# Kernel optimization log

Hardware: AMD Instinct MI355X
Metric: run time of the kernel (lower is better)

## Reference

```python
import jax, jax.numpy as jnp
import numpy as np

J = 24  # fixed pooling window (SampleLength/N = 1200/50)


def setup_inputs() -> dict:
    key = jax.random.key(0)
    k1, k2, k3 = jax.random.split(key, 3)
    T, N, K, C = 786432, 50, 400, 10  # T = 32768 segments * J
    x = jax.random.normal(k1, (T, N), dtype=jnp.float32)
    W1 = jax.random.normal(k2, (K, N), dtype=jnp.float32) * 0.1
    W2 = jax.random.normal(k3, (C, K), dtype=jnp.float32) * 0.1
    return {"x": x, "W1": W1, "W2": W2}


def reference(x, W1, W2):
    # linear + relu: [T, N] @ [N, K] -> [T, K]
    local_features = jax.nn.relu(jnp.einsum('tn,kn->tk', x, W1))
    # fixed-window mean over consecutive J rows: [T, K] -> [T//J, K]
    T, K = local_features.shape
    features = local_features.reshape(T // J, J, K).mean(axis=1)
    # final linear: [T//J, K] @ [K, C] -> [T//J, C]
    logits = jnp.einsum('bk,ck->bc', features, W2)
    return logits
```

## Files before the change

### kernel.cpp

```cpp
#include <hip/hip_runtime.h>
#include <hip/hip_bf16.h>

#define T_TOTAL 786432
#define N_IN 50
#define K_FEAT 400
#define C_OUT 10
#define NSEG 32768

#define W1F_TASKS (25 * 2 * 64)
#define W2T_OFF_BYTES 51200
#define W2T_FLOATS (25 * 320)
#define W2F_OFF_BYTES 83200
#define W2F_TASKS (13 * 64)
#define W1F32_OFF_BYTES 98304
#define W1F32_TASKS (13 * 4 * 64)
#define PREP_TASKS (W1F_TASKS + W2T_FLOATS + W2F_TASKS + W1F32_TASKS)
#define POOLED_OFF_BYTES 163840
#define POOLED_STRIDE 416
#define WS_NEEDED (POOLED_OFF_BYTES + (size_t)NSEG * POOLED_STRIDE * 2)

typedef __bf16 bfx8 __attribute__((ext_vector_type(8)));
typedef short  s16x8 __attribute__((ext_vector_type(8)));
typedef float  f32x4 __attribute__((ext_vector_type(4)));
typedef float  f32x16 __attribute__((ext_vector_type(16)));

static __device__ __forceinline__ short f2bf(float f) {
    union { float f; unsigned u; } v; v.f = f;
    unsigned r = v.u + 0x7fffu + ((v.u >> 16) & 1u);
    return (short)(r >> 16);
}

__global__ void prep_kernel(const float* __restrict__ W1,
                            const float* __restrict__ W2,
                            short* __restrict__ w1f, float* __restrict__ w2t,
                            short* __restrict__ w2f, short* __restrict__ w1f32)
{
    const int gid = blockIdx.x * blockDim.x + threadIdx.x;
    if (gid < W1F_TASKS) {
        const int lane = gid & 63;
        const int s    = (gid >> 6) & 1;
        const int tile = gid >> 7;
        const int m16  = lane & 15;
        const int quad = lane >> 4;
        const float* row = W1 + (tile * 16 + m16) * N_IN;
        s16x8 v;
        #pragma unroll
        for (int j = 0; j < 8; ++j) {
            const int n = s * 32 + quad * 8 + j;
            v[j] = (n < N_IN) ? f2bf(row[n]) : (short)0;
        }
        *(s16x8*)&w1f[gid * 8] = v;
    } else if (gid < W1F_TASKS + W2T_FLOATS) {
        const int i   = gid - W1F_TASKS;
        const int j   = i / 320;
        const int tid = i - j * 320;
        const int o    = tid >> 4;
        const int part = tid & 15;
        const int seg  = (o >= 10) ? 1 : 0;
        const int cls  = o - seg * 10;
        w2t[i] = W2[cls * K_FEAT + part * 25 + j];
    } else if (gid < W1F_TASKS + W2T_FLOATS + W2F_TASKS) {
        const int i    = gid - W1F_TASKS - W2T_FLOATS;
        const int lane = i & 63;
        const int kt   = i >> 6;
        const int m16  = lane & 15;
        const int quad = lane >> 4;
        s16x8 v;
        #pragma unroll
        for (int j = 0; j < 8; ++j) {
            const int feat = kt * 32 + quad * 8 + j;
            v[j] = (m16 < C_OUT && feat < K_FEAT) ? f2bf(W2[m16 * K_FEAT + feat])
                                                  : (short)0;
        }
        *(s16x8*)&w2f[i * 8] = v;
    } else if (gid < PREP_TASKS) {
        const int i    = gid - W1F_TASKS - W2T_FLOATS - W2F_TASKS;
        const int lane = i & 63;
        const int fi   = i >> 6;
        const int ft   = fi >> 2;
        const int kt   = fi & 3;
        const int feat = ft * 32 + (lane & 31);
        const int cbase = kt * 16 + (lane >> 5) * 8;
        s16x8 v;
        #pragma unroll
        for (int j = 0; j < 8; ++j) {
            const int col = cbase + j;
            v[j] = (feat < K_FEAT && col < N_IN) ? f2bf(W1[feat * N_IN + col])
                                                 : (short)0;
        }
        *(s16x8*)&w1f32[i * 8] = v;
    }
}

__global__ __launch_bounds__(256, 4) void phase1_kernel(
    const float* __restrict__ x, const short* __restrict__ w1f32,
    short* __restrict__ pooled)
{
    const int tid  = threadIdx.x;
    const int lane = tid & 63;
    const int m32  = lane & 31;
    const int h    = lane >> 5;
    const int chunk = blockIdx.x * 4 + (tid >> 6);
    const s16x8* wf = (const s16x8*)w1f32;

    s16x8 Af[3][4];
    {
        const float* xg = x + (size_t)chunk * (96 * N_IN);
        #pragma unroll
        for (int rt = 0; rt < 3; ++rt) {
            const float* rp = xg + (32 * rt + m32) * N_IN;
            #pragma unroll
            for (int kt = 0; kt < 3; ++kt) {
                const float* p = rp + 16 * kt + 8 * h;
                s16x8 f;
                #pragma unroll
                for (int q = 0; q < 4; ++q) {
                    const float2 u = *(const float2*)(p + 2 * q);
                    f[2 * q]     = f2bf(u.x);
                    f[2 * q + 1] = f2bf(u.y);
                }
                Af[rt][kt] = f;
            }
            s16x8 f3 = {0, 0, 0, 0, 0, 0, 0, 0};
            if (h == 0) {
                const float2 u = *(const float2*)(rp + 48);
                f3[0] = f2bf(u.x); f3[1] = f2bf(u.y);
            }
            Af[rt][3] = f3;
        }
    }

    const int segbase = chunk * 4;

    s16x8 Bc[4], Bn[4];
    #pragma unroll
    for (int kt = 0; kt < 4; ++kt) Bc[kt] = wf[kt * 64 + lane];

    for (int ft = 0; ft < 13; ++ft) {
        const int ftn = (ft < 12) ? ft + 1 : 12;
        #pragma unroll
        for (int kt = 0; kt < 4; ++kt) Bn[kt] = wf[(ftn * 4 + kt) * 64 + lane];

        float s0 = 0.f, s1 = 0.f, s2 = 0.f, s3 = 0.f;
        #pragma unroll
        for (int rt = 0; rt < 3; ++rt) {
            f32x16 acc;
            #pragma unroll
            for (int r = 0; r < 16; ++r) acc[r] = 0.f;
            #pragma unroll
            for (int kt = 0; kt < 4; ++kt)
                acc = __builtin_amdgcn_mfma_f32_32x32x16_bf16(
                        __builtin_bit_cast(bfx8, Af[rt][kt]),
                        __builtin_bit_cast(bfx8, Bc[kt]), acc, 0, 0, 0);
            float c0 = 0.f, c1 = 0.f;
            #pragma unroll
            for (int r = 0; r < 16; ++r) {
                const float v = fmaxf(acc[r], 0.f);
                if ((r >> 2) < 3 - rt) c0 += v; else c1 += v;
            }
            if (rt == 0)      { s0 += c0; s1 += c1; }
            else if (rt == 1) { s1 += c0; s2 += c1; }
            else              { s2 += c0; s3 += c1; }
        }
        s0 += __shfl_xor(s0, 32);
        s1 += __shfl_xor(s1, 32);
        s2 += __shfl_xor(s2, 32);
        s3 += __shfl_xor(s3, 32);
        if (lane < 32) {
            const size_t fo = 32 * ft + lane;
            pooled[(size_t)(segbase + 0) * POOLED_STRIDE + fo] = f2bf(s0);
            pooled[(size_t)(segbase + 1) * POOLED_STRIDE + fo] = f2bf(s1);
            pooled[(size_t)(segbase + 2) * POOLED_STRIDE + fo] = f2bf(s2);
            pooled[(size_t)(segbase + 3) * POOLED_STRIDE + fo] = f2bf(s3);
        }
        #pragma unroll
        for (int kt = 0; kt < 4; ++kt) Bc[kt] = Bn[kt];
    }
}

__global__ __launch_bounds__(256) void phase2_kernel(
    const short* __restrict__ pooled, const short* __restrict__ w2f,
    float* __restrict__ out)
{
    const int tid  = threadIdx.x;
    const int lane = tid & 63;
    const int m16  = lane & 15;
    const int quad = lane >> 4;
    const int segbase = (blockIdx.x * 4 + (tid >> 6)) * 16;
    const s16x8* wf = (const s16x8*)w2f;
    const short* arow = pooled + (size_t)(segbase + m16) * POOLED_STRIDE;

    f32x4 acc = {0.f, 0.f, 0.f, 0.f};
    s16x8 zero = {0, 0, 0, 0, 0, 0, 0, 0};
    #pragma unroll
    for (int kt = 0; kt < 13; ++kt) {
        const s16x8 b = wf[kt * 64 + lane];
        const s16x8 a = (kt == 12 && quad >= 2)
                            ? zero
                            : *(const s16x8*)(arow + kt * 32 + quad * 8);
        acc = __builtin_amdgcn_mfma_f32_16x16x32_bf16(
                __builtin_bit_cast(bfx8, a), __builtin_bit_cast(bfx8, b),
                acc, 0, 0, 0);
    }
    if (m16 < C_OUT) {
        #pragma unroll
        for (int rg = 0; rg < 4; ++rg)
            out[(size_t)(segbase + quad * 4 + rg) * C_OUT + m16] =
                acc[rg] * (1.0f / 24.0f);
    }
}

#define FB_CPB 4
#define FB_NTHREADS 320
#define FB_XS_STRIDE 72
#define FB_XS_ROWS (FB_CPB * 48)

__global__ __launch_bounds__(FB_NTHREADS) void classifier_fb(
    const float* __restrict__ x, const short* __restrict__ w1f,
    const float* __restrict__ w2t, float* __restrict__ out)
{
    __shared__ short xs[FB_XS_ROWS * FB_XS_STRIDE];
    __shared__ float pooled[2 * K_FEAT];

    const int tid  = threadIdx.x;
    const int wave = tid >> 6;
    const int lane = tid & 63;
    const int m16  = lane & 15;
    const int quad = lane >> 4;

    {
        const float* xb = x + (size_t)blockIdx.x * (FB_XS_ROWS * N_IN);
        #pragma unroll
        for (int it = 0; it < (FB_XS_ROWS * 25) / FB_NTHREADS; ++it) {
            const int i = tid + it * FB_NTHREADS;
            const int r = i / 25;
            const int c2 = i - r * 25;
            const float2 v = *(const float2*)(xb + 2 * i);
            const int packed = (unsigned short)f2bf(v.x) |
                               ((unsigned)(unsigned short)f2bf(v.y) << 16);
            *(int*)&xs[r * FB_XS_STRIDE + 2 * c2] = packed;
        }
        for (int i = tid; i < FB_XS_ROWS * 7; i += FB_NTHREADS) {
            const int r = i / 7;
            const int c = 50 + 2 * (i - r * 7);
            *(int*)&xs[r * FB_XS_STRIDE + c] = 0;
        }
    }

    s16x8 bfrag[5][2];
    {
        const s16x8* wf = (const s16x8*)w1f;
        #pragma unroll
        for (int t = 0; t < 5; ++t)
            #pragma unroll
            for (int s = 0; s < 2; ++s)
                bfrag[t][s] = wf[((wave * 5 + t) * 2 + s) * 64 + lane];
    }

    const int o    = tid >> 4;
    const int part = tid & 15;
    const int segO = (o >= 10) ? 1 : 0;
    const int cls  = o - segO * 10;
    float w2r[25];
    #pragma unroll
    for (int j = 0; j < 25; ++j) w2r[j] = w2t[j * FB_NTHREADS + tid];

    __syncthreads();

    for (int ciq = 0; ciq < FB_CPB; ++ciq) {
        s16x8 a[3][2];
        #pragma unroll
        for (int r = 0; r < 3; ++r) {
            const short* arow =
                &xs[(ciq * 48 + r * 16 + m16) * FB_XS_STRIDE + quad * 8];
            a[r][0] = *(const s16x8*)(arow);
            a[r][1] = *(const s16x8*)(arow + 32);
        }
        #pragma unroll
        for (int t = 0; t < 5; ++t) {
            float c0 = 0.f, c1 = 0.f;
            #pragma unroll
            for (int r = 0; r < 3; ++r) {
                f32x4 acc = {0.f, 0.f, 0.f, 0.f};
                acc = __builtin_amdgcn_mfma_f32_16x16x32_bf16(
                        __builtin_bit_cast(bfx8, a[r][0]),
                        __builtin_bit_cast(bfx8, bfrag[t][0]), acc, 0, 0, 0);
                acc = __builtin_amdgcn_mfma_f32_16x16x32_bf16(
                        __builtin_bit_cast(bfx8, a[r][1]),
                        __builtin_bit_cast(bfx8, bfrag[t][1]), acc, 0, 0, 0);
                const float s = fmaxf(acc[0], 0.f) + fmaxf(acc[1], 0.f)
                              + fmaxf(acc[2], 0.f) + fmaxf(acc[3], 0.f);
                if (r * 4 + quad < 6) c0 += s; else c1 += s;
            }
            c0 += __shfl_xor(c0, 16); c0 += __shfl_xor(c0, 32);
            c1 += __shfl_xor(c1, 16); c1 += __shfl_xor(c1, 32);
            if (quad == 0) {
                const int feat = (wave * 5 + t) * 16 + m16;
                pooled[feat] = c0;
                pooled[K_FEAT + feat] = c1;
            }
        }
        __syncthreads();

        float sum = 0.f;
        const float* pv = &pooled[segO * K_FEAT + part * 25];
        #pragma unroll
        for (int j = 0; j < 25; ++j) sum += pv[j] * w2r[j];
        sum += __shfl_down(sum, 8, 16);
        sum += __shfl_down(sum, 4, 16);
        sum += __shfl_down(sum, 2, 16);
        sum += __shfl_down(sum, 1, 16);
        if (part == 0) {
            const int chunk = blockIdx.x * FB_CPB + ciq;
            out[(chunk * 2 + segO) * C_OUT + cls] = sum * (1.0f / 24.0f);
        }
        __syncthreads();
    }
}

extern "C" void kernel_launch(void* const* d_in, const int* in_sizes, int n_in,
                              void* d_out, int out_size, void* d_ws, size_t ws_size,
                              hipStream_t stream) {
    const float* x  = (const float*)d_in[0];
    const float* W1 = (const float*)d_in[1];
    const float* W2 = (const float*)d_in[2];
    float* out = (float*)d_out;

    short* w1f   = (short*)d_ws;
    float* w2t   = (float*)((char*)d_ws + W2T_OFF_BYTES);
    short* w2f   = (short*)((char*)d_ws + W2F_OFF_BYTES);
    short* w1f32 = (short*)((char*)d_ws + W1F32_OFF_BYTES);
    short* pooled = (short*)((char*)d_ws + POOLED_OFF_BYTES);

    prep_kernel<<<(PREP_TASKS + 255) / 256, 256, 0, stream>>>(W1, W2, w1f, w2t,
                                                              w2f, w1f32);

    if (ws_size >= WS_NEEDED) {
        phase1_kernel<<<2048, 256, 0, stream>>>(x, w1f32, pooled);
        phase2_kernel<<<512, 256, 0, stream>>>(pooled, w2f, out);
    } else {
        classifier_fb<<<4096, FB_NTHREADS, 0, stream>>>(x, w1f, w2t, out);
    }
}
```

Measured before the change: 260.7 us.

## Fuse classifier into phase1 and stage x through LDS with packed bf16 convert

Drops the pooled intermediate buffer and the separate phase2 kernel. Each wave now multiplies its pooled sums by fp32 W2 slices and reduces across lanes with shuffles before writing the logits. The x tile is loaded with coalesced float4 reads, converted with v_cvt_pk_bf16_f32, staged in LDS, and then read back as MFMA fragments. This saves a global round trip and a kernel launch. In exchange it adds 38KB of LDS per block, which may limit occupancy, plus extra FMA and shuffle work.

```diff
diff --git a/kernel.cpp b/kernel.cpp
--- a/kernel.cpp
+++ b/kernel.cpp
@@ -10,14 +10,12 @@
 #define W1F_TASKS (25 * 2 * 64)
 #define W2T_OFF_BYTES 51200
 #define W2T_FLOATS (25 * 320)
-#define W2F_OFF_BYTES 83200
-#define W2F_TASKS (13 * 64)
 #define W1F32_OFF_BYTES 98304
 #define W1F32_TASKS (13 * 4 * 64)
-#define PREP_TASKS (W1F_TASKS + W2T_FLOATS + W2F_TASKS + W1F32_TASKS)
-#define POOLED_OFF_BYTES 163840
-#define POOLED_STRIDE 416
-#define WS_NEEDED (POOLED_OFF_BYTES + (size_t)NSEG * POOLED_STRIDE * 2)
+#define W2P_OFF_BYTES 163840
+#define W2P_TASKS (13 * 64)
+#define PREP_TASKS (W1F_TASKS + W2T_FLOATS + W1F32_TASKS + W2P_TASKS)
+#define WS_NEEDED (W2P_OFF_BYTES + (size_t)W2P_TASKS * 8 * 4)
 
 typedef __bf16 bfx8 __attribute__((ext_vector_type(8)));
 typedef short  s16x8 __attribute__((ext_vector_type(8)));
@@ -33,7 +31,7 @@
 __global__ void prep_kernel(const float* __restrict__ W1,
                             const float* __restrict__ W2,
                             short* __restrict__ w1f, float* __restrict__ w2t,
-                            short* __restrict__ w2f, short* __restrict__ w1f32)
+                            short* __restrict__ w1f32, float* __restrict__ w2p)
 {
     const int gid = blockIdx.x * blockDim.x + threadIdx.x;
     if (gid < W1F_TASKS) {
@@ -59,22 +57,8 @@
         const int seg  = (o >= 10) ? 1 : 0;
         const int cls  = o - seg * 10;
         w2t[i] = W2[cls * K_FEAT + part * 25 + j];
-    } else if (gid < W1F_TASKS + W2T_FLOATS + W2F_TASKS) {
+    } else if (gid < W1F_TASKS + W2T_FLOATS + W1F32_TASKS) {
         const int i    = gid - W1F_TASKS - W2T_FLOATS;
-        const int lane = i & 63;
-        const int kt   = i >> 6;
-        const int m16  = lane & 15;
-        const int quad = lane >> 4;
-        s16x8 v;
-        #pragma unroll
-        for (int j = 0; j < 8; ++j) {
-            const int feat = kt * 32 + quad * 8 + j;
-            v[j] = (m16 < C_OUT && feat < K_FEAT) ? f2bf(W2[m16 * K_FEAT + feat])
-                                                  : (short)0;
-        }
-        *(s16x8*)&w2f[i * 8] = v;
-    } else if (gid < PREP_TASKS) {
-        const int i    = gid - W1F_TASKS - W2T_FLOATS - W2F_TASKS;
         const int lane = i & 63;
         const int fi   = i >> 6;
         const int ft   = fi >> 2;
@@ -89,48 +73,83 @@
                                                  : (short)0;
         }
         *(s16x8*)&w1f32[i * 8] = v;
+    } else if (gid < PREP_TASKS) {
+        const int i    = gid - W1F_TASKS - W2T_FLOATS - W1F32_TASKS;
+        const int lane = i & 63;
+        const int ft   = i >> 6;
+        const int m32  = lane & 31;
+        const int h    = lane >> 5;
+        const int feat = 32 * ft + m32;
+        float v[8];
+        #pragma unroll
+        for (int c = 0; c < 8; ++c)
+            v[c] = (c < 5 && feat < K_FEAT) ? W2[(h * 5 + c) * K_FEAT + feat]
+                                            : 0.f;
+        float4* dst = (float4*)&w2p[(size_t)i * 8];
+        dst[0] = make_float4(v[0], v[1], v[2], v[3]);
+        dst[1] = make_float4(v[4], v[5], v[6], v[7]);
     }
 }
 
 __global__ __launch_bounds__(256, 4) void phase1_kernel(
     const float* __restrict__ x, const short* __restrict__ w1f32,
-    short* __restrict__ pooled)
+    const float* __restrict__ w2p, float* __restrict__ out)
 {
+    __shared__ __align__(16) short xs[4 * 4800];
     const int tid  = threadIdx.x;
     const int lane = tid & 63;
+    const int wv   = tid >> 6;
     const int m32  = lane & 31;
     const int h    = lane >> 5;
-    const int chunk = blockIdx.x * 4 + (tid >> 6);
+    const int chunk = blockIdx.x * 4 + wv;
+    short* myxs = xs + wv * 4800;
+
+    {
+        const float* xg = x + (size_t)chunk * 4800;
+        #pragma unroll
+        for (int i = 0; i < 19; ++i) {
+            const int q = 64 * i + lane;
+            if (i < 18 || lane < 48) {
+                const float4 v = *(const float4*)(xg + 4 * q);
+                int lo, hi;
+                asm("v_cvt_pk_bf16_f32 %0, %1, %2" : "=v"(lo) : "v"(v.x), "v"(v.y));
+                asm("v_cvt_pk_bf16_f32 %0, %1, %2" : "=v"(hi) : "v"(v.z), "v"(v.w));
+                int2 pk; pk.x = lo; pk.y = hi;
+                *(int2*)&myxs[4 * q] = pk;
+            }
+        }
+    }
+    asm volatile("s_waitcnt lgkmcnt(0)" ::: "memory");
+    __builtin_amdgcn_sched_barrier(0);
+
+    s16x8 Af[3][4];
+    #pragma unroll
+    for (int rt = 0; rt < 3; ++rt) {
+        const int row = 32 * rt + m32;
+        const short* rp = myxs + row * 50 + 8 * h;
+        #pragma unroll
+        for (int kt = 0; kt < 3; ++kt) {
+            int d0 = *(const int*)(rp + 16 * kt + 0);
+            int d1 = *(const int*)(rp + 16 * kt + 2);
+            int d2 = *(const int*)(rp + 16 * kt + 4);
+            int d3 = *(const int*)(rp + 16 * kt + 6);
+            int4 di = {d0, d1, d2, d3};
+            Af[rt][kt] = __builtin_bit_cast(s16x8, di);
+        }
+        int dt = 0;
+        if (h == 0) dt = *(const int*)(myxs + row * 50 + 48);
+        int4 di3 = {dt, 0, 0, 0};
+        Af[rt][3] = __builtin_bit_cast(s16x8, di3);
+    }
+
+    const int segbase = chunk * 4;
     const s16x8* wf = (const s16x8*)w1f32;
 
-    s16x8 Af[3][4];
-    {
-        const float* xg = x + (size_t)chunk * (96 * N_IN);
-        #pragma unroll
-        for (int rt = 0; rt < 3; ++rt) {
-            const float* rp = xg + (32 * rt + m32) * N_IN;
-            #pragma unroll
-            for (int kt = 0; kt < 3; ++kt) {
-                const float* p = rp + 16 * kt + 8 * h;
-                s16x8 f;
-                #pragma unroll
-                for (int q = 0; q < 4; ++q) {
-                    const float2 u = *(const float2*)(p + 2 * q);
-                    f[2 * q]     = f2bf(u.x);
-                    f[2 * q + 1] = f2bf(u.y);
-                }
-                Af[rt][kt] = f;
-            }
-            s16x8 f3 = {0, 0, 0, 0, 0, 0, 0, 0};
-            if (h == 0) {
-                const float2 u = *(const float2*)(rp + 48);
-                f3[0] = f2bf(u.x); f3[1] = f2bf(u.y);
-            }
-            Af[rt][3] = f3;
-        }
-    }
-
-    const int segbase = chunk * 4;
+    float oacc[4][5];
+    #pragma unroll
+    for (int s = 0; s < 4; ++s)
+        #pragma unroll
+        for (int c = 0; c < 5; ++c) oacc[s][c] = 0.f;
 
     s16x8 Bc[4], Bn[4];
     #pragma unroll
@@ -166,47 +185,42 @@
         s1 += __shfl_xor(s1, 32);
         s2 += __shfl_xor(s2, 32);
         s3 += __shfl_xor(s3, 32);
-        if (lane < 32) {
-            const size_t fo = 32 * ft + lane;
-            pooled[(size_t)(segbase + 0) * POOLED_STRIDE + fo] = f2bf(s0);
-            pooled[(size_t)(segbase + 1) * POOLED_STRIDE + fo] = f2bf(s1);
-            pooled[(size_t)(segbase + 2) * POOLED_STRIDE + fo] = f2bf(s2);
-            pooled[(size_t)(segbase + 3) * POOLED_STRIDE + fo] = f2bf(s3);
+
+        {
+            const float* wl = w2p + (size_t)(ft * 64 + lane) * 8;
+            const float4 wa = *(const float4*)wl;
+            const float  w4 = wl[4];
+            const float wc[5] = {wa.x, wa.y, wa.z, wa.w, w4};
+            const float sv[4] = {s0, s1, s2, s3};
+            #pragma unroll
+            for (int s = 0; s < 4; ++s)
+                #pragma unroll
+                for (int c = 0; c < 5; ++c)
+                    oacc[s][c] = fmaf(sv[s], wc[c], oacc[s][c]);
         }
         #pragma unroll
         for (int kt = 0; kt < 4; ++kt) Bc[kt] = Bn[kt];
     }
-}
-
-__global__ __launch_bounds__(256) void phase2_kernel(
-    const short* __restrict__ pooled, const short* __restrict__ w2f,
-    float* __restrict__ out)
-{
-    const int tid  = threadIdx.x;
-    const int lane = tid & 63;
-    const int m16  = lane & 15;
-    const int quad = lane >> 4;
-    const int segbase = (blockIdx.x * 4 + (tid >> 6)) * 16;
-    const s16x8* wf = (const s16x8*)w2f;
-    const short* arow = pooled + (size_t)(segbase + m16) * POOLED_STRIDE;
-
-    f32x4 acc = {0.f, 0.f, 0.f, 0.f};
-    s16x8 zero = {0, 0, 0, 0, 0, 0, 0, 0};
-    #pragma unroll
-    for (int kt = 0; kt < 13; ++kt) {
-        const s16x8 b = wf[kt * 64 + lane];
-        const s16x8 a = (kt == 12 && quad >= 2)
-                            ? zero
-                            : *(const s16x8*)(arow + kt * 32 + quad * 8);
-        acc = __builtin_amdgcn_mfma_f32_16x16x32_bf16(
-                __builtin_bit_cast(bfx8, a), __builtin_bit_cast(bfx8, b),
-                acc, 0, 0, 0);
-    }
-    if (m16 < C_OUT) {
-        #pragma unroll
-        for (int rg = 0; rg < 4; ++rg)
-            out[(size_t)(segbase + quad * 4 + rg) * C_OUT + m16] =
-                acc[rg] * (1.0f / 24.0f);
+
+    #pragma unroll
+    for (int s = 0; s < 4; ++s)
+        #pragma unroll
+        for (int c = 0; c < 5; ++c) {
+            float v = oacc[s][c];
+            v += __shfl_xor(v, 1);
+            v += __shfl_xor(v, 2);
+            v += __shfl_xor(v, 4);
+            v += __shfl_xor(v, 8);
+            v += __shfl_xor(v, 16);
+            oacc[s][c] = v;
+        }
+    if (m32 == 0) {
+        #pragma unroll
+        for (int s = 0; s < 4; ++s)
+            #pragma unroll
+            for (int c = 0; c < 5; ++c)
+                out[(size_t)(segbase + s) * C_OUT + h * 5 + c] =
+                    oacc[s][c] * (1.0f / 24.0f);
     }
 }
 
@@ -328,16 +342,14 @@
 
     short* w1f   = (short*)d_ws;
     float* w2t   = (float*)((char*)d_ws + W2T_OFF_BYTES);
-    short* w2f   = (short*)((char*)d_ws + W2F_OFF_BYTES);
     short* w1f32 = (short*)((char*)d_ws + W1F32_OFF_BYTES);
-    short* pooled = (short*)((char*)d_ws + POOLED_OFF_BYTES);
+    float* w2p   = (float*)((char*)d_ws + W2P_OFF_BYTES);
 
     prep_kernel<<<(PREP_TASKS + 255) / 256, 256, 0, stream>>>(W1, W2, w1f, w2t,
-                                                              w2f, w1f32);
+                                                              w1f32, w2p);
 
     if (ws_size >= WS_NEEDED) {
-        phase1_kernel<<<2048, 256, 0, stream>>>(x, w1f32, pooled);
-        phase2_kernel<<<512, 256, 0, stream>>>(pooled, w2f, out);
+        phase1_kernel<<<2048, 256, 0, stream>>>(x, w1f32, w2p, out);
     } else {
         classifier_fb<<<4096, FB_NTHREADS, 0, stream>>>(x, w1f, w2t, out);
     }
```

Result: slower. 277.0 us (+6.3%).
